# Optimization experiments

Measured on AMD Instinct MI355X. Metric: run time of the kernel, lower is better.

Reference implementation:

```python
import jax, jax.numpy as jnp
import numpy as np

H, KVH, D = 32, 8, 128          # query heads, kv heads, head dim
HID = H * D                      # 4096
N_REP = H // KVH
HEAVY_RATIO, RECENT_RATIO = 0.1, 0.1
B, S = 1, 2048


def setup_inputs() -> dict:
    key = jax.random.key(0)
    ks = jax.random.split(key, 8)
    scale = 0.02
    hidden_states = jax.random.normal(ks[0], (B, S, HID), jnp.float32)
    neg = jnp.finfo(jnp.float32).min
    causal = jnp.where(jnp.tril(jnp.ones((S, S), bool)), 0.0, neg)
    attention_mask = jnp.broadcast_to(causal[None, None], (B, 1, S, S)).astype(jnp.float32)
    return {
        "hidden_states": hidden_states,
        "attention_mask": attention_mask,
        "Wq": jax.random.normal(ks[1], (HID, H * D), jnp.float32) * scale,
        "bq": jax.random.normal(ks[2], (H * D,), jnp.float32) * scale,
        "Wk": jax.random.normal(ks[3], (HID, KVH * D), jnp.float32) * scale,
        "bk": jax.random.normal(ks[4], (KVH * D,), jnp.float32) * scale,
        "Wv": jax.random.normal(ks[5], (HID, KVH * D), jnp.float32) * scale,
        "bv": jax.random.normal(ks[6], (KVH * D,), jnp.float32) * scale,
        "Wo": jax.random.normal(ks[7], (H * D, HID), jnp.float32) * scale,
    }


def reference(hidden_states, attention_mask, Wq, bq, Wk, bk, Wv, bv, Wo):
    b, s, _ = hidden_states.shape
    # QKV projections (q/k/v have bias, o does not)
    q = (hidden_states @ Wq + bq).reshape(b, s, H, D).transpose(0, 2, 1, 3)      # [B,H,S,D]
    k = (hidden_states @ Wk + bk).reshape(b, s, KVH, D).transpose(0, 2, 1, 3)    # [B,KVH,S,D]
    v = (hidden_states @ Wv + bv).reshape(b, s, KVH, D).transpose(0, 2, 1, 3)
    # repeat_kv: head h uses kv head h // N_REP (matches expand+reshape order)
    k = jnp.repeat(k, N_REP, axis=1)                                             # [B,H,S,D]
    v = jnp.repeat(v, N_REP, axis=1)
    scores = jnp.einsum('bhqd,bhkd->bhqk', q, k) / jnp.sqrt(jnp.asarray(D, q.dtype))
    neg = jnp.finfo(scores.dtype).min
    scores = jnp.maximum(scores + attention_mask, neg)
    attn = jax.nn.softmax(scores.astype(jnp.float32), axis=-1).astype(q.dtype)   # [B,H,S,S]
    # H2O: accumulate per-key scores (first step: no previous_scores)
    cur_scores = attn.sum(axis=0).sum(axis=1)                                    # [H, S]
    heavy_budget = int(HEAVY_RATIO * s)
    recent_budget = int(RECENT_RATIO * s)
    # cache_budget = heavy + recent < s, so eviction branch always runs here
    mask = jnp.ones((H, s + 1), attn.dtype)
    mask = mask.at[:, : s + 1 - recent_budget].set(0.0)
    selected = cur_scores[:, : s - recent_budget]                                # exclude recent window
    _, topk_idx = jax.lax.top_k(selected, heavy_budget)                          # [H, heavy]
    mask = jax.vmap(lambda m, i: m.at[i].set(1.0))(mask, topk_idx)               # scatter heavy hitters
    attention_masks_next = mask[None, :, None, :]                                # [1,H,1,S+1]
    score_mask = mask[:, :-1].at[:, -recent_budget:].set(1.0)
    new_scores = cur_scores * score_mask                                         # evicted scores zeroed
    # attention output
    out = jnp.einsum('bhqk,bhkd->bhqd', attn, v)                                 # [B,H,S,D]
    out = out.transpose(0, 2, 1, 3).reshape(b, s, HID) @ Wo
    return out, attention_masks_next, new_scores
```

## Files before the change

kernel.cpp:

```cpp
#include <hip/hip_runtime.h>
#include <stdint.h>

#define SEQ 2048
#define HID 4096
#define KVHID 1024
#define NHEAD 32
#define DHEAD 128
#define HEAVY 204
#define SEL_N 1844

typedef float f32x4 __attribute__((ext_vector_type(4)));
typedef __bf16 bf16x8 __attribute__((ext_vector_type(8)));

#define MFMA16 __builtin_amdgcn_mfma_f32_16x16x32_bf16

__device__ __forceinline__ unsigned short f2bf(float x) {
    unsigned int u = __float_as_uint(x);
    u = (u + 0x7fffu + ((u >> 16) & 1u)) >> 16;
    return (unsigned short)u;
}
__device__ __forceinline__ float bf2f(unsigned short s) {
    return __uint_as_float(((unsigned int)s) << 16);
}
__device__ __forceinline__ unsigned long long pack4(unsigned short a, unsigned short b,
                                                    unsigned short c, unsigned short d) {
    return (unsigned long long)a | ((unsigned long long)b << 16) |
           ((unsigned long long)c << 32) | ((unsigned long long)d << 48);
}
__device__ __forceinline__ float fexp2(float x) {
#if __has_builtin(__builtin_amdgcn_exp2f)
    return __builtin_amdgcn_exp2f(x);
#else
    float r; asm volatile("v_exp_f32 %0, %1\ns_nop 1" : "=v"(r) : "v"(x)); return r;
#endif
}
__device__ __forceinline__ unsigned cvt_pk_bf16(float lo, float hi) {
    unsigned r; asm("v_cvt_pk_bf16_f32 %0, %1, %2" : "=v"(r) : "v"(lo), "v"(hi)); return r;
}
__device__ __forceinline__ void gload_lds16(const unsigned short* g, unsigned short* l) {
    __builtin_amdgcn_global_load_lds(
        (const __attribute__((address_space(1))) void*)g,
        (__attribute__((address_space(3))) void*)l, 16, 0, 0);
}
__device__ __forceinline__ void block_sync() {
    asm volatile("" ::: "memory");
    __builtin_amdgcn_s_barrier();
    asm volatile("" ::: "memory");
}

template<bool SPLIT>
__device__ __forceinline__ void wprep_body(const float* __restrict__ W,
    unsigned short* __restrict__ Thi, unsigned short* __restrict__ Tlo,
    int K, int N, int bx, int by, float (*T)[65])
{
    const int k0 = by << 6, n0 = bx << 6;
    const int tid = threadIdx.x;
    const int c = tid & 63, r4 = tid >> 6;
    #pragma unroll
    for (int i = 0; i < 16; ++i)
        T[r4 + i * 4][c] = W[(size_t)(k0 + r4 + i * 4) * N + n0 + c];
    __syncthreads();
    #pragma unroll
    for (int i = 0; i < 16; ++i) {
        const int n = r4 + i * 4;
        const float x = T[c][n];
        const size_t o = (size_t)(n0 + n) * K + k0 + c;
        const unsigned short h = f2bf(x);
        Thi[o] = h;
        if constexpr (SPLIT) Tlo[o] = f2bf(x - bf2f(h));
    }
}

__global__ __launch_bounds__(256) void prep_all(
    const float* __restrict__ hidden,
    unsigned short* __restrict__ hs_hi, unsigned short* __restrict__ hs_lo,
    const float* __restrict__ Wq, unsigned short* __restrict__ wqT_hi,
    unsigned short* __restrict__ wqT_lo,
    const float* __restrict__ Wk, unsigned short* __restrict__ wkT_hi,
    unsigned short* __restrict__ wkT_lo,
    const float* __restrict__ Wv, unsigned short* __restrict__ wvT)
{
    __shared__ float T[64][65];
    const int bid = blockIdx.x;
    if (bid < 2048) {
        const int n4 = (SEQ * HID) / 4;
        int i = bid * 256 + threadIdx.x;
        for (; i < n4; i += 2048 * 256) {
            const float4 v = ((const float4*)hidden)[i];
            const unsigned short h0 = f2bf(v.x), h1 = f2bf(v.y),
                                 h2 = f2bf(v.z), h3 = f2bf(v.w);
            ((unsigned long long*)hs_hi)[i] = pack4(h0, h1, h2, h3);
            ((unsigned long long*)hs_lo)[i] =
                pack4(f2bf(v.x - bf2f(h0)), f2bf(v.y - bf2f(h1)),
                      f2bf(v.z - bf2f(h2)), f2bf(v.w - bf2f(h3)));
        }
    } else if (bid < 6144) {
        const int idx = bid - 2048;
        wprep_body<true>(Wq, wqT_hi, wqT_lo, HID, HID, idx & 63, idx >> 6, T);
    } else if (bid < 7168) {
        const int idx = bid - 6144;
        wprep_body<true>(Wk, wkT_hi, wkT_lo, HID, KVHID, idx & 15, idx >> 4, T);
    } else {
        const int idx = bid - 7168;
        wprep_body<false>(Wv, wvT, nullptr, HID, KVHID, idx & 15, idx >> 4, T);
    }
}

template<bool SPLIT>
__global__ __launch_bounds__(256) void wprep(const float* __restrict__ W,
    unsigned short* __restrict__ Thi, unsigned short* __restrict__ Tlo, int K, int N)
{
    __shared__ float T[64][65];
    wprep_body<SPLIT>(W, Thi, Tlo, K, N, blockIdx.x, blockIdx.y, T);
}

template<bool SPLIT, int OUTMODE , bool BIAS>
__device__ __forceinline__ void gemm_body(
    const unsigned short* __restrict__ Ahi, const unsigned short* __restrict__ Alo,
    const unsigned short* __restrict__ Bhi, const unsigned short* __restrict__ Blo,
    const float* __restrict__ bias,
    void* __restrict__ C0, unsigned short* __restrict__ C1,
    int M, int N, int K, int mb, int nb, unsigned short* sm)
{
    constexpr int NT = SPLIT ? 4 : 2;
    const int tid = threadIdx.x;
    const int l = tid & 63, w = tid >> 6;
    const int lr = l & 15, lg = l >> 4;
    const int wm = (w >> 1) * 64, wn = (w & 1) * 64;
    const int m0 = mb * 128, n0 = nb * 128;

    const unsigned short* aH = Ahi + (size_t)m0 * K;
    const unsigned short* bH = Bhi + (size_t)n0 * K;
    const unsigned short* aL = SPLIT ? Alo + (size_t)m0 * K : nullptr;
    const unsigned short* bL = SPLIT ? Blo + (size_t)n0 * K : nullptr;

    const int s0_ = tid, s1_ = tid + 256;
    const int r0_ = s0_ >> 2, c0_ = (s0_ & 3) ^ (r0_ & 3);
    const int r1_ = s1_ >> 2, c1_ = (s1_ & 3) ^ (r1_ & 3);
    const size_t g0off = (size_t)r0_ * K + c0_ * 8;
    const size_t g1off = (size_t)r1_ * K + c1_ * 8;

#define GB_SLOT(buf, t) (sm + ((buf) * NT + (t)) * 4096)
#define GB_STAGE(buf, kk)                                                       \
    do {                                                                        \
        const int k0s = (kk) << 5;                                              \
        gload_lds16(aH + g0off + k0s, GB_SLOT(buf, 0) + s0_ * 8);               \
        gload_lds16(aH + g1off + k0s, GB_SLOT(buf, 0) + s1_ * 8);               \
        gload_lds16(bH + g0off + k0s, GB_SLOT(buf, 1) + s0_ * 8);               \
        gload_lds16(bH + g1off + k0s, GB_SLOT(buf, 1) + s1_ * 8);               \
        if constexpr (SPLIT) {                                                  \
            gload_lds16(aL + g0off + k0s, GB_SLOT(buf, 2) + s0_ * 8);           \
            gload_lds16(aL + g1off + k0s, GB_SLOT(buf, 2) + s1_ * 8);           \
            gload_lds16(bL + g0off + k0s, GB_SLOT(buf, 3) + s0_ * 8);           \
            gload_lds16(bL + g1off + k0s, GB_SLOT(buf, 3) + s1_ * 8);           \
        }                                                                       \
    } while (0)

#define GB_COMPUTE(BC)                                                          \
    do {                                                                        \
        bf16x8 ah[4], bh[4], al[4], bl[4];                                      \
        _Pragma("unroll")                                                       \
        for (int mi = 0; mi < 4; ++mi) {                                        \
            const int rr = wm + mi * 16 + lr;                                   \
            const int o = rr * 32 + ((lg ^ (rr & 3)) << 3);                     \
            ah[mi] = *(const bf16x8*)(GB_SLOT(BC, 0) + o);                      \
            if constexpr (SPLIT) al[mi] = *(const bf16x8*)(GB_SLOT(BC, 2) + o); \
        }                                                                       \
        _Pragma("unroll")                                                       \
        for (int ni = 0; ni < 4; ++ni) {                                        \
            const int rr = wn + ni * 16 + lr;                                   \
            const int o = rr * 32 + ((lg ^ (rr & 3)) << 3);                     \
            bh[ni] = *(const bf16x8*)(GB_SLOT(BC, 1) + o);                      \
            if constexpr (SPLIT) bl[ni] = *(const bf16x8*)(GB_SLOT(BC, 3) + o); \
        }                                                                       \
        __builtin_amdgcn_s_setprio(1);                                          \
        _Pragma("unroll")                                                       \
        for (int mi = 0; mi < 4; ++mi)                                          \
            _Pragma("unroll")                                                   \
            for (int ni = 0; ni < 4; ++ni) {                                    \
                acc[mi][ni] = MFMA16(ah[mi], bh[ni], acc[mi][ni], 0, 0, 0);     \
                if constexpr (SPLIT) {                                          \
                    acc[mi][ni] = MFMA16(ah[mi], bl[ni], acc[mi][ni], 0, 0, 0); \
                    acc[mi][ni] = MFMA16(al[mi], bh[ni], acc[mi][ni], 0, 0, 0); \
                }                                                               \
            }                                                                   \
        __builtin_amdgcn_s_setprio(0);                                          \
    } while (0)

    f32x4 acc[4][4];
    #pragma unroll
    for (int i = 0; i < 4; ++i)
        #pragma unroll
        for (int j = 0; j < 4; ++j) acc[i][j] = (f32x4){};

    const int nk = K >> 5;
    if constexpr (SPLIT) {
        GB_STAGE(0, 0);
        for (int kt = 0; kt < nk; ++kt) {
            if (kt + 1 < nk) {
                GB_STAGE((kt + 1) & 1, kt + 1);
                asm volatile("s_waitcnt vmcnt(8)" ::: "memory");
            } else {
                asm volatile("s_waitcnt vmcnt(0)" ::: "memory");
            }
            block_sync();
            GB_COMPUTE(kt & 1);
            block_sync();
        }
    } else {
        GB_STAGE(0, 0);
        GB_STAGE(1, 1);
        for (int kt = 0; kt < nk; ++kt) {
            if (kt + 2 < nk) {
                GB_STAGE((kt + 2) & 3, kt + 2);
                asm volatile("s_waitcnt vmcnt(8)" ::: "memory");
            } else if (kt + 1 < nk) {
                asm volatile("s_waitcnt vmcnt(4)" ::: "memory");
            } else {
                asm volatile("s_waitcnt vmcnt(0)" ::: "memory");
            }
            block_sync();
            GB_COMPUTE(kt & 3);
        }
    }
#undef GB_STAGE
#undef GB_COMPUTE
#undef GB_SLOT

    #pragma unroll
    for (int ni = 0; ni < 4; ++ni) {
        const int col = n0 + wn + ni * 16 + lr;
        float bv = 0.f;
        if constexpr (BIAS) bv = bias[col];
        #pragma unroll
        for (int mi = 0; mi < 4; ++mi) {
            #pragma unroll
            for (int r = 0; r < 4; ++r) {
                const int row = m0 + wm + mi * 16 + lg * 4 + r;
                const float x = acc[mi][ni][r] + bv;
                const size_t o = (size_t)row * N + col;
                if constexpr (OUTMODE == 1) {
                    ((float*)C0)[o] = x;
                } else if constexpr (OUTMODE == 0) {
                    ((unsigned short*)C0)[o] = f2bf(x);
                } else {
                    const unsigned short hi = f2bf(x);
                    ((unsigned short*)C0)[o] = hi;
                    C1[o] = f2bf(x - bf2f(hi));
                }
            }
        }
    }
}

__global__ __launch_bounds__(256) void qkv_gemm(
    const unsigned short* __restrict__ hs_hi, const unsigned short* __restrict__ hs_lo,
    const unsigned short* __restrict__ wqT_hi, const unsigned short* __restrict__ wqT_lo,
    const unsigned short* __restrict__ wkT_hi, const unsigned short* __restrict__ wkT_lo,
    const unsigned short* __restrict__ wvT,
    const float* __restrict__ bq, const float* __restrict__ bk, const float* __restrict__ bv,
    unsigned short* __restrict__ q_hi, unsigned short* __restrict__ q_lo,
    unsigned short* __restrict__ k_hi, unsigned short* __restrict__ k_lo,
    unsigned short* __restrict__ v_bf)
{
    __shared__ unsigned short sm[8 * 4096];
    const int bid = blockIdx.x;
    if (bid < 512) {
        const int r = bid & 7, rid = bid >> 3;
        const int mb = ((r >> 2) << 3) + (rid >> 3);
        const int nb = ((r & 3) << 3) + (rid & 7);
        gemm_body<true, 2, true>(hs_hi, hs_lo, wqT_hi, wqT_lo, bq, q_hi, q_lo,
                                 SEQ, HID, HID, mb, nb, sm);
    } else if (bid < 640) {
        const int idx = bid - 512;
        gemm_body<true, 2, true>(hs_hi, hs_lo, wkT_hi, wkT_lo, bk, k_hi, k_lo,
                                 SEQ, KVHID, HID, idx >> 3, idx & 7, sm);
    } else {
        const int idx = bid - 640;
        gemm_body<false, 0, true>(hs_hi, nullptr, wvT, nullptr, bv, v_bf, nullptr,
                                  SEQ, KVHID, HID, idx >> 3, idx & 7, sm);
    }
}

__global__ __launch_bounds__(256) void gemm_wo(
    const unsigned short* __restrict__ A, const unsigned short* __restrict__ B,
    float* __restrict__ C, int M, int N, int K)
{
    __shared__ unsigned short sm[8 * 4096];
    gemm_body<false, 1, false>(A, nullptr, B, nullptr, nullptr, C, nullptr,
                               M, N, K, blockIdx.y, blockIdx.x, sm);
}

__global__ __launch_bounds__(256) void transpose_v(const unsigned short* __restrict__ v,
                                                   unsigned short* __restrict__ vt)
{
    __shared__ unsigned short T[64][65];
    const int r0 = blockIdx.x * 64;
    const int c0 = blockIdx.y * 64;
    const int tid = threadIdx.x;
    const int cc = tid & 63, rr = tid >> 6;
    #pragma unroll
    for (int i = 0; i < 16; ++i)
        T[rr + i * 4][cc] = v[(size_t)(r0 + rr + i * 4) * KVHID + c0 + cc];
    __syncthreads();
    #pragma unroll
    for (int i = 0; i < 16; ++i) {
        const int oc = rr + i * 4;
        vt[(size_t)(c0 + oc) * SEQ + r0 + cc] = T[cc][oc];
    }
}

__device__ __forceinline__ void stage_tile(
    const unsigned short* __restrict__ khi, const unsigned short* __restrict__ klo,
    unsigned short* kb, int kt, int kvoff, int w, int lane)
{
    const unsigned short* src = (w >> 1) ? klo : khi;
    unsigned short* dst = kb + (w >> 1) * 4096 + (w & 1) * 2048;
    const int lsub = lane >> 4;
    const int lbyte = (lane & 15) * 16;
    #pragma unroll
    for (int j = 0; j < 4; ++j) {
        const int row = (w & 1) * 16 + j * 4 + lsub;
        const int soff = (lbyte ^ ((row & 7) << 4)) >> 1;
        const unsigned short* g = src + (size_t)(kt * 32 + row) * KVHID + kvoff + soff;
        gload_lds16(g, dst + j * 512);
    }
}

__device__ __forceinline__ void process_qblock8(
    int head, int qb, int w, int lane,
    const unsigned short* __restrict__ qhi, const unsigned short* __restrict__ qlo,
    const unsigned short* __restrict__ khi, const unsigned short* __restrict__ klo,
    const unsigned short* __restrict__ vT,
    unsigned short* __restrict__ obuf, double* __restrict__ colsum,
    unsigned short* kbuf , unsigned short* pl)
{
    const int lr = lane & 15, lg = lane >> 4;
    const int kvoff = (head >> 2) * DHEAD;
    const int q0w = qb * 64 + w * 16;
    const int NT = 2 * qb + 2;
    const int wnt = ((q0w + 15) >> 5) + 1;
    const float C = 0.08838834764831845f * 1.44269504088896340f;

    bf16x8 qh[4], qlo4[4];
    {
        const size_t qbase = (size_t)(q0w + lr) * HID + head * DHEAD + lg * 8;
        #pragma unroll
        for (int s = 0; s < 4; ++s) {
            qh[s]   = *(const bf16x8*)(qhi + qbase + s * 32);
            qlo4[s] = *(const bf16x8*)(qlo + qbase + s * 32);
        }
    }
    const int swz = (lr & 7) << 3;

    float rl[4];
    {
        float lp[4] = {0.f, 0.f, 0.f, 0.f};
        stage_tile(khi, klo, kbuf, 0, kvoff, w, lane);
        stage_tile(khi, klo, kbuf + 8192, 1, kvoff, w, lane);
        for (int kt = 0; kt < NT; ++kt) {
            if (kt + 2 < NT) {
                stage_tile(khi, klo, kbuf + ((kt + 2) & 3) * 8192, kt + 2, kvoff, w, lane);
                asm volatile("s_waitcnt vmcnt(8)" ::: "memory");
            } else if (kt + 1 < NT) {
                asm volatile("s_waitcnt vmcnt(4)" ::: "memory");
            } else {
                asm volatile("s_waitcnt vmcnt(0)" ::: "memory");
            }
            block_sync();
            const unsigned short* kb = kbuf + (kt & 3) * 8192;
            if (kt < wnt) {
                f32x4 m0 = {}, m1 = {}, xa0 = {}, xb0 = {}, xa1 = {}, xb1 = {};
                #pragma unroll
                for (int s = 0; s < 4; ++s) {
                    const int d = s * 32 + lg * 8;
                    const bf16x8 k0h = *(const bf16x8*)(kb + (lr * 128 + (d ^ swz)));
                    const bf16x8 k1h = *(const bf16x8*)(kb + ((16 + lr) * 128 + (d ^ swz)));
                    const bf16x8 k0l = *(const bf16x8*)(kb + 4096 + lr * 128 + (d ^ swz));
                    const bf16x8 k1l = *(const bf16x8*)(kb + 4096 + (16 + lr) * 128 + (d ^ swz));
                    m0  = MFMA16(qh[s],   k0h, m0,  0, 0, 0);
                    m1  = MFMA16(qh[s],   k1h, m1,  0, 0, 0);
                    xa0 = MFMA16(qh[s],   k0l, xa0, 0, 0, 0);
                    xb0 = MFMA16(qlo4[s], k0h, xb0, 0, 0, 0);
                    xa1 = MFMA16(qh[s],   k1l, xa1, 0, 0, 0);
                    xb1 = MFMA16(qlo4[s], k1h, xb1, 0, 0, 0);
                }
                const bool full = (kt * 32 + 31 <= q0w);
                #pragma unroll
                for (int r = 0; r < 4; ++r) {
                    float e0 = fexp2((m0[r] + (xa0[r] + xb0[r])) * C);
                    float e1 = fexp2((m1[r] + (xa1[r] + xb1[r])) * C);
                    if (!full) {
                        const int q = q0w + lg * 4 + r;
                        if (kt * 32 + lr > q)      e0 = 0.f;
                        if (kt * 32 + 16 + lr > q) e1 = 0.f;
                    }
                    lp[r] += e0 + e1;
                }
            }
        }
        block_sync();
        #pragma unroll
        for (int r = 0; r < 4; ++r) {
            float v = lp[r];
            v += __shfl_xor(v, 1);
            v += __shfl_xor(v, 2);
            v += __shfl_xor(v, 4);
            v += __shfl_xor(v, 8);
            rl[r] = 1.0f / v;
        }
    }
    {
        f32x4 oacc[8];
        #pragma unroll
        for (int f = 0; f < 8; ++f) oacc[f] = (f32x4){};
        stage_tile(khi, klo, kbuf, 0, kvoff, w, lane);
        stage_tile(khi, klo, kbuf + 8192, 1, kvoff, w, lane);
        for (int kt = 0; kt < NT; ++kt) {
            if (kt + 2 < NT) {
                stage_tile(khi, klo, kbuf + ((kt + 2) & 3) * 8192, kt + 2, kvoff, w, lane);
                asm volatile("s_waitcnt vmcnt(8)" ::: "memory");
            } else if (kt + 1 < NT) {
                asm volatile("s_waitcnt vmcnt(4)" ::: "memory");
            } else {
                asm volatile("s_waitcnt vmcnt(0)" ::: "memory");
            }
            block_sync();
            const unsigned short* kb = kbuf + (kt & 3) * 8192;
            if (kt < wnt) {
                f32x4 m0 = {}, m1 = {}, xa0 = {}, xb0 = {}, xa1 = {}, xb1 = {};
                #pragma unroll
                for (int s = 0; s < 4; ++s) {
                    const int d = s * 32 + lg * 8;
                    const bf16x8 k0h = *(const bf16x8*)(kb + (lr * 128 + (d ^ swz)));
                    const bf16x8 k1h = *(const bf16x8*)(kb + ((16 + lr) * 128 + (d ^ swz)));
                    const bf16x8 k0l = *(const bf16x8*)(kb + 4096 + lr * 128 + (d ^ swz));
                    const bf16x8 k1l = *(const bf16x8*)(kb + 4096 + (16 + lr) * 128 + (d ^ swz));
                    m0  = MFMA16(qh[s],   k0h, m0,  0, 0, 0);
                    m1  = MFMA16(qh[s],   k1h, m1,  0, 0, 0);
                    xa0 = MFMA16(qh[s],   k0l, xa0, 0, 0, 0);
                    xb0 = MFMA16(qlo4[s], k0h, xb0, 0, 0, 0);
                    xa1 = MFMA16(qh[s],   k1l, xa1, 0, 0, 0);
                    xb1 = MFMA16(qlo4[s], k1h, xb1, 0, 0, 0);
                }
                const bool full = (kt * 32 + 31 <= q0w);
                float p0[4], p1[4];
                float cs0 = 0.f, cs1 = 0.f;
                #pragma unroll
                for (int r = 0; r < 4; ++r) {
                    float e0 = fexp2((m0[r] + (xa0[r] + xb0[r])) * C);
                    float e1 = fexp2((m1[r] + (xa1[r] + xb1[r])) * C);
                    if (!full) {
                        const int q = q0w + lg * 4 + r;
                        if (kt * 32 + lr > q)      e0 = 0.f;
                        if (kt * 32 + 16 + lr > q) e1 = 0.f;
                    }
                    p0[r] = e0 * rl[r];
                    p1[r] = e1 * rl[r];
                    cs0 += p0[r];
                    cs1 += p1[r];
                }
                cs0 += __shfl_xor(cs0, 16); cs0 += __shfl_xor(cs0, 32);
                cs1 += __shfl_xor(cs1, 16); cs1 += __shfl_xor(cs1, 32);
                if (lg == 0) {
                    atomicAdd(&colsum[head * SEQ + kt * 32 + lr], (double)cs0);
                    atomicAdd(&colsum[head * SEQ + kt * 32 + 16 + lr], (double)cs1);
                }
                #pragma unroll
                for (int r = 0; r < 4; r += 2) {
                    const int row0 = (lg * 4 + r) * 40;
                    unsigned u0 = cvt_pk_bf16(p0[r], p0[r + 1]);
                    unsigned u1 = cvt_pk_bf16(p1[r], p1[r + 1]);
                    pl[row0 + lr]      = (unsigned short)u0;
                    pl[row0 + 40 + lr] = (unsigned short)(u0 >> 16);
                    pl[row0 + 16 + lr] = (unsigned short)u1;
                    pl[row0 + 56 + lr] = (unsigned short)(u1 >> 16);
                }
                const bf16x8 pa = *(const bf16x8*)(pl + lr * 40 + lg * 8);
                #pragma unroll
                for (int f = 0; f < 8; ++f) {
                    const bf16x8 vf = *(const bf16x8*)(vT + (size_t)(kvoff + f * 16 + lr) * SEQ
                                                       + kt * 32 + lg * 8);
                    oacc[f] = MFMA16(pa, vf, oacc[f], 0, 0, 0);
                }
            }
        }
        block_sync();
        #pragma unroll
        for (int f = 0; f < 8; ++f)
            #pragma unroll
            for (int r = 0; r < 4; ++r)
                obuf[(size_t)(q0w + lg * 4 + r) * HID + head * DHEAD + f * 16 + lr] =
                    f2bf(oacc[f][r]);
    }
}

__global__ __launch_bounds__(256) void attn_fused8(
    const unsigned short* __restrict__ qhi, const unsigned short* __restrict__ qlo,
    const unsigned short* __restrict__ khi, const unsigned short* __restrict__ klo,
    const unsigned short* __restrict__ vT,
    unsigned short* __restrict__ obuf, double* __restrict__ colsum)
{
    __shared__ unsigned short kbuf[4][2 * 4096];
    __shared__ unsigned short plds[4][16 * 40];
    const int head = blockIdx.x >> 4;
    const int pr = blockIdx.x & 15;
    const int tid = threadIdx.x;
    const int w = tid >> 6, lane = tid & 63;
    process_qblock8(head, pr, w, lane, qhi, qlo, khi, klo, vT, obuf, colsum,
                    &kbuf[0][0], &plds[w][0]);
    process_qblock8(head, 31 - pr, w, lane, qhi, qlo, khi, klo, vT, obuf, colsum,
                    &kbuf[0][0], &plds[w][0]);
}

__global__ __launch_bounds__(256) void topk_kernel(const double* __restrict__ colsum,
                                                   float* __restrict__ outbuf)
{
    __shared__ float sc[SEL_N];
    __shared__ unsigned char fl[SEL_N];
    __shared__ int cnt;
    const int h = blockIdx.x;
    const int tid = threadIdx.x;
    for (int j = tid; j < SEL_N; j += 256) {
        sc[j] = (float)colsum[h * SEQ + j];
        fl[j] = 0;
    }
    __syncthreads();
    unsigned int cand = 0u;
    for (int b = 30; b >= 0; --b) {
        const unsigned int t = cand | (1u << b);
        const float tv = __uint_as_float(t);
        if (tid == 0) cnt = 0;
        __syncthreads();
        int local = 0;
        for (int j = tid; j < SEL_N; j += 256) local += (sc[j] >= tv) ? 1 : 0;
        atomicAdd(&cnt, local);
        __syncthreads();
        if (cnt >= HEAVY) cand = t;
        __syncthreads();
    }
    const float v204 = __uint_as_float(cand);
    if (tid == 0) cnt = 0;
    __syncthreads();
    int local = 0;
    for (int j = tid; j < SEL_N; j += 256) {
        if (sc[j] > v204) { fl[j] = 1; local++; }
    }
    atomicAdd(&cnt, local);
    __syncthreads();
    if (tid == 0) {
        int need = HEAVY - cnt;
        for (int j = 0; j < SEL_N && need > 0; ++j) {
            if (sc[j] == v204) { fl[j] = 1; --need; }
        }
    }
    __syncthreads();
    float* mask_out = outbuf + 8388608 + h * 2049;
    float* score_out = outbuf + 8388608 + NHEAD * 2049 + h * SEQ;
    for (int j = tid; j < 2049; j += 256) {
        float mv;
        if (j >= 1845) mv = 1.f;
        else if (j < SEL_N) mv = fl[j] ? 1.f : 0.f;
        else mv = 0.f;
        mask_out[j] = mv;
    }
    for (int j = tid; j < SEQ; j += 256) {
        const float cur = (float)colsum[h * SEQ + j];
        const float smv = (j >= SEL_N) ? 1.f : (fl[j] ? 1.f : 0.f);
        score_out[j] = cur * smv;
    }
}

extern "C" void kernel_launch(void* const* d_in, const int* in_sizes, int n_in,
                              void* d_out, int out_size, void* d_ws, size_t ws_size,
                              hipStream_t stream)
{
    const float* hidden = (const float*)d_in[0];
    const float* Wq = (const float*)d_in[2];
    const float* bq = (const float*)d_in[3];
    const float* Wk = (const float*)d_in[4];
    const float* bk = (const float*)d_in[5];
    const float* Wv = (const float*)d_in[6];
    const float* bv = (const float*)d_in[7];
    const float* Wo = (const float*)d_in[8];
    float* out = (float*)d_out;

    char* ws = (char*)d_ws;
    unsigned short* hs_hi = (unsigned short*)(ws);
    unsigned short* hs_lo = (unsigned short*)(ws + 16777216ull);
    unsigned short* wqT_hi = (unsigned short*)(ws + 33554432ull);
    unsigned short* wqT_lo = (unsigned short*)(ws + 67108864ull);
    unsigned short* wkT_hi = (unsigned short*)(ws + 100663296ull);
    unsigned short* wkT_lo = (unsigned short*)(ws + 109051904ull);
    unsigned short* wvT    = (unsigned short*)(ws + 117440512ull);
    unsigned short* q_hi   = (unsigned short*)(ws + 125829120ull);
    unsigned short* q_lo   = (unsigned short*)(ws + 142606336ull);
    unsigned short* k_hi   = (unsigned short*)(ws + 159383552ull);
    unsigned short* k_lo   = (unsigned short*)(ws + 163577856ull);
    unsigned short* v_bf   = (unsigned short*)(ws + 167772160ull);
    unsigned short* vT     = (unsigned short*)(ws + 171966464ull);
    unsigned short* o_bf   = (unsigned short*)(ws + 176160768ull);
    double* colsum         = (double*)(ws + 192937984ull);
    unsigned short* woT    = wqT_hi;

    dim3 blk(256);
    prep_all<<<dim3(8192), blk, 0, stream>>>(
        hidden, hs_hi, hs_lo, Wq, wqT_hi, wqT_lo, Wk, wkT_hi, wkT_lo, Wv, wvT);

    qkv_gemm<<<dim3(768), blk, 0, stream>>>(
        hs_hi, hs_lo, wqT_hi, wqT_lo, wkT_hi, wkT_lo, wvT,
        bq, bk, bv, q_hi, q_lo, k_hi, k_lo, v_bf);

    transpose_v<<<dim3(32, 16), blk, 0, stream>>>(v_bf, vT);
    (void)hipMemsetAsync((void*)colsum, 0, (size_t)NHEAD * SEQ * sizeof(double), stream);
    attn_fused8<<<dim3(512), blk, 0, stream>>>(q_hi, q_lo, k_hi, k_lo, vT, o_bf, colsum);
    topk_kernel<<<dim3(32), blk, 0, stream>>>(colsum, out);

    wprep<false><<<dim3(64, 64), blk, 0, stream>>>(Wo, woT, nullptr, HID, HID);
    gemm_wo<<<dim3(32, 16), blk, 0, stream>>>(o_bf, woT, out, SEQ, HID, HID);
}
```

Measured before the change: 787.8 us.

## Fold colsum zeroing and Wo transpose into prep kernel; swizzle Wo GEMM tiles

Zeroing of the column-sum buffer and the Wo transpose/bf16 conversion move into the merged prep_all launch when the workspace is large enough. This removes a separate memset and a separate wprep launch. gemm_wo switches to a 1D grid with a block swizzle that groups tiles into 2x4 regions of 8x8 tiles, aiming for better L2 reuse. It needs an extra 32MB workspace region, with a fallback to the old aliased path when the workspace is too small.

```diff
diff --git a/kernel.cpp b/kernel.cpp
--- a/kernel.cpp
+++ b/kernel.cpp
@@ -78,7 +78,9 @@
     unsigned short* __restrict__ wqT_lo,
     const float* __restrict__ Wk, unsigned short* __restrict__ wkT_hi,
     unsigned short* __restrict__ wkT_lo,
-    const float* __restrict__ Wv, unsigned short* __restrict__ wvT)
+    const float* __restrict__ Wv, unsigned short* __restrict__ wvT,
+    double* __restrict__ colsum,
+    const float* __restrict__ Wo, unsigned short* __restrict__ woT)
 {
     __shared__ float T[64][65];
     const int bid = blockIdx.x;
@@ -100,9 +102,17 @@
     } else if (bid < 7168) {
         const int idx = bid - 6144;
         wprep_body<true>(Wk, wkT_hi, wkT_lo, HID, KVHID, idx & 15, idx >> 4, T);
-    } else {
+    } else if (bid < 8192) {
         const int idx = bid - 7168;
         wprep_body<false>(Wv, wvT, nullptr, HID, KVHID, idx & 15, idx >> 4, T);
+    } else if (bid < 8256) {
+        unsigned long long* p = (unsigned long long*)colsum;
+        const int n = NHEAD * SEQ;
+        for (int i = (bid - 8192) * 256 + threadIdx.x; i < n; i += 64 * 256)
+            p[i] = 0ull;
+    } else {
+        const int idx = bid - 8256;
+        wprep_body<false>(Wo, woT, nullptr, HID, HID, idx & 63, idx >> 6, T);
     }
 }
 
@@ -287,8 +297,12 @@
     float* __restrict__ C, int M, int N, int K)
 {
     __shared__ unsigned short sm[8 * 4096];
+    const int bid = blockIdx.x;
+    const int r = bid & 7, rid = bid >> 3;
+    const int mb = ((r >> 2) << 3) + (rid >> 3);
+    const int nb = ((r & 3) << 3) + (rid & 7);
     gemm_body<false, 1, false>(A, nullptr, B, nullptr, nullptr, C, nullptr,
-                               M, N, K, blockIdx.y, blockIdx.x, sm);
+                               M, N, K, mb, nb, sm);
 }
 
 __global__ __launch_bounds__(256) void transpose_v(const unsigned short* __restrict__ v,
@@ -601,21 +615,28 @@
     unsigned short* vT     = (unsigned short*)(ws + 171966464ull);
     unsigned short* o_bf   = (unsigned short*)(ws + 176160768ull);
     double* colsum         = (double*)(ws + 192937984ull);
-    unsigned short* woT    = wqT_hi;
-
+    unsigned short* woT2   = (unsigned short*)(ws + 193462272ull);
+    unsigned short* woT_alias = wqT_hi;
+
+    const bool bigws = ws_size >= (193462272ull + 33554432ull);
     dim3 blk(256);
-    prep_all<<<dim3(8192), blk, 0, stream>>>(
-        hidden, hs_hi, hs_lo, Wq, wqT_hi, wqT_lo, Wk, wkT_hi, wkT_lo, Wv, wvT);
+
+    prep_all<<<dim3(bigws ? 12352 : 8256), blk, 0, stream>>>(
+        hidden, hs_hi, hs_lo, Wq, wqT_hi, wqT_lo, Wk, wkT_hi, wkT_lo, Wv, wvT,
+        colsum, Wo, woT2);
 
     qkv_gemm<<<dim3(768), blk, 0, stream>>>(
         hs_hi, hs_lo, wqT_hi, wqT_lo, wkT_hi, wkT_lo, wvT,
         bq, bk, bv, q_hi, q_lo, k_hi, k_lo, v_bf);
 
     transpose_v<<<dim3(32, 16), blk, 0, stream>>>(v_bf, vT);
-    (void)hipMemsetAsync((void*)colsum, 0, (size_t)NHEAD * SEQ * sizeof(double), stream);
     attn_fused8<<<dim3(512), blk, 0, stream>>>(q_hi, q_lo, k_hi, k_lo, vT, o_bf, colsum);
     topk_kernel<<<dim3(32), blk, 0, stream>>>(colsum, out);
 
-    wprep<false><<<dim3(64, 64), blk, 0, stream>>>(Wo, woT, nullptr, HID, HID);
-    gemm_wo<<<dim3(32, 16), blk, 0, stream>>>(o_bf, woT, out, SEQ, HID, HID);
-}
+    const unsigned short* woT = woT2;
+    if (!bigws) {
+        wprep<false><<<dim3(64, 64), blk, 0, stream>>>(Wo, woT_alias, nullptr, HID, HID);
+        woT = woT_alias;
+    }
+    gemm_wo<<<dim3(512), blk, 0, stream>>>(o_bf, woT, out, SEQ, HID, HID);
+}
```

Result: no change. 791.8 us (+0.5%).
